# Performance work log

Measured on AMD Instinct MI355X. Metric: run time of the kernel, lower is better.

Reference implementation:

```python
import jax, jax.numpy as jnp
import numpy as np

# ---- config constants (must match init_kwargs) ----
B, S, D, H, HD = 2, 2048, 512, 8, 64
N_BLK, L_BLK = 64, 32          # block_size, block_len (S = N_BLK*L_BLK)
R, RM = 8, 4                   # router_size, group_router_mul_factor
LN, GN, GE, GT = 8, 4, 16, 2   # moe layers, groups, group experts, topk per token
DR, DG = 128, 128
FFH = 1024
THETA = 10000.0
EPS = 1e-6

_INV_FREQ = (1.0 / THETA) ** (np.arange(0, HD, 2, dtype=np.float32) / HD)


def rmsnorm(x, w):
    return x * jax.lax.rsqrt(jnp.mean(x * x, axis=-1, keepdims=True) + EPS) * w


def rope(x):
    # x: (b, h, s, hd); y1 = x1*cos + x2*sin, y2 = -x1*sin + x2*cos (as in RotaryEmb)
    s = x.shape[2]
    freqs = jnp.outer(jnp.arange(s, dtype=jnp.float32), jnp.asarray(_INV_FREQ))[None, None]
    cos, sin = jnp.cos(freqs), jnp.sin(freqs)
    x1, x2 = jnp.split(x, 2, axis=-1)
    return jnp.concatenate([x1 * cos + x2 * sin, -x1 * sin + x2 * cos], axis=-1)


def layer(x, mask, qkv_w, o_w, up_w, down_w, n1, n2):
    b, s, d = x.shape
    xn = rmsnorm(x, n1)
    q, k, v = jnp.split(xn @ qkv_w, 3, axis=-1)
    sh = lambda t: t.reshape(b, s, H, HD).transpose(0, 2, 1, 3)  # b h s hd
    q, k, v = rope(sh(q)), rope(sh(k)), sh(v)
    scores = jnp.einsum('bhqa,bhka->bhqk', q, k) / np.sqrt(HD).astype(np.float32)
    if mask is not None:
        scores = jnp.where(mask[:, None], scores, -jnp.inf)
    p = jax.nn.softmax(scores, axis=-1)
    o = jnp.einsum('bhqk,bhka->bhqa', p, v).transpose(0, 2, 1, 3).reshape(b, s, d)
    x = x + o @ o_w
    xn2 = rmsnorm(x, n2)
    h1, h2 = jnp.split(xn2 @ up_w, 2, axis=-1)
    return x + (jax.nn.silu(h1) * h2) @ down_w


def _l2n(t, axis):
    return t / jnp.maximum(jnp.linalg.norm(t, axis=axis, keepdims=True), 1e-12)


def forward(x, doc, router_token, out_w, keys_router, keys_gate,
            enc_qkv, enc_o, enc_up, enc_down, enc_n1, enc_n2,
            rtr_qkv, rtr_o, rtr_up, rtr_down, rtr_n1, rtr_n2):
    # ---- AuxEncoder: block-causal AND same-document mask (global_attn branch) ----
    qb = jnp.arange(S) // N_BLK
    causal = qb[:, None] >= qb[None, :]                       # (S, S)
    mask = causal[None] & (doc[:, :, None] == doc[:, None, :])  # (B, S, S)
    for i in range(enc_qkv.shape[0]):
        x = layer(x, mask, enc_qkv[i], enc_o[i], enc_up[i], enc_down[i], enc_n1[i], enc_n2[i])

    # ---- AuxRouter: split into blocks, append router tokens, full attention ----
    xr = x.reshape(B * L_BLK, N_BLK, D)
    rt = jnp.broadcast_to(router_token, (B * L_BLK, R, D))
    xr = jnp.concatenate([xr, rt], axis=1)                    # (B*L, N+R, D)
    for i in range(rtr_qkv.shape[0]):
        xr = layer(xr, None, rtr_qkv[i], rtr_o[i], rtr_up[i], rtr_down[i], rtr_n1[i], rtr_n2[i])
    out = xr[:, N_BLK:] @ out_w                               # (B*L, R, DR+DG)
    xro, xgo = out[..., :DR], out[..., DR:]

    def expand(t, dd):
        # repeat '(b l) r d -> (r rm) b l d', roll(1, dim=2), flatten(1,2)
        t = t.reshape(B, L_BLK, R, dd).transpose(2, 0, 1, 3)  # (R, B, L, d)
        t = jnp.repeat(t, RM, axis=0)                          # (R*RM, B, L, d)
        t = jnp.roll(t, 1, axis=2)
        return t.reshape(R * RM, B * L_BLK, dd)

    xrr = _l2n(expand(xro, DR), -1)
    xgg = _l2n(expand(xgo, DG), -1)
    kr = _l2n(keys_router, 1)
    kg = _l2n(keys_gate, 1)
    rl = jnp.einsum('gbd,gde->gbe', xrr, kr)                  # (LN*GN, B*L, GE)
    gl = jnp.einsum('gbd,gde->gbe', xgg, kg)
    _, idx = jax.lax.top_k(rl, GT)                            # (LN*GN, B*L, GT)
    rv = jnp.take_along_axis(rl, idx, axis=-1)
    gv = jnp.take_along_axis(gl, idx, axis=-1)
    return jnp.stack([rv, gv], axis=0)                        # (2, 32, 64, 2)


def setup_inputs() -> dict:
    key = jax.random.key(0)
    ks = jax.random.split(key, 20)
    w = lambda k, shp: 0.02 * jax.random.normal(k, shp, dtype=jnp.float32)
    return {
        'x': jax.random.normal(ks[0], (B, S, D), dtype=jnp.float32),
        'doc': jnp.sort(jax.random.randint(ks[1], (B, S), 0, 4), axis=-1),
        'router_token': jax.random.normal(ks[2], (1, R, D), dtype=jnp.float32),
        'out_w': w(ks[3], (D, DR + DG)),
        'keys_router': jax.random.normal(ks[4], (LN * GN, DR, GE), dtype=jnp.float32),
        'keys_gate': jax.random.normal(ks[5], (LN * GN, DG, GE), dtype=jnp.float32),
        'enc_qkv': w(ks[6], (4, D, 3 * D)),
        'enc_o': w(ks[7], (4, D, D)),
        'enc_up': w(ks[8], (4, D, 2 * FFH)),
        'enc_down': w(ks[9], (4, FFH, D)),
        'enc_n1': jnp.ones((4, D), dtype=jnp.float32),
        'enc_n2': jnp.ones((4, D), dtype=jnp.float32),
        'rtr_qkv': w(ks[10], (2, D, 3 * D)),
        'rtr_o': w(ks[11], (2, D, D)),
        'rtr_up': w(ks[12], (2, D, 2 * FFH)),
        'rtr_down': w(ks[13], (2, FFH, D)),
        'rtr_n1': jnp.ones((2, D), dtype=jnp.float32),
        'rtr_n2': jnp.ones((2, D), dtype=jnp.float32),
    }


def reference(x, doc, router_token, out_w, keys_router, keys_gate,
              enc_qkv, enc_o, enc_up, enc_down, enc_n1, enc_n2,
              rtr_qkv, rtr_o, rtr_up, rtr_down, rtr_n1, rtr_n2):
    return forward(x, doc, router_token, out_w, keys_router, keys_gate,
                   enc_qkv, enc_o, enc_up, enc_down, enc_n1, enc_n2,
                   rtr_qkv, rtr_o, rtr_up, rtr_down, rtr_n1, rtr_n2)
```

## Files before the change

### kernel.cpp

```cpp
#include <hip/hip_runtime.h>
#include <hip/hip_bf16.h>
#include <cstdint>


typedef __attribute__((ext_vector_type(8))) short short8;
typedef __attribute__((ext_vector_type(4))) float f32x4;
typedef unsigned short ushort_t;

__device__ __forceinline__ float bf2f(unsigned short u) {
    return __uint_as_float(((unsigned)u) << 16);
}
__device__ __forceinline__ unsigned short f2bf(float f) {
    unsigned u = __float_as_uint(f);
    unsigned r = 0x7FFFu + ((u >> 16) & 1u);
    return (unsigned short)((u + r) >> 16);
}
__device__ __forceinline__ float wave_sum64(float v) {
#pragma unroll
    for (int o = 32; o; o >>= 1) v += __shfl_xor(v, o);
    return v;
}
__device__ __forceinline__ void load_lds16(const ushort_t* g, ushort_t* l) {
    __builtin_amdgcn_global_load_lds(
        (const __attribute__((address_space(1))) unsigned int*)g,
        (__attribute__((address_space(3))) unsigned int*)l, 16, 0, 0);
}

#define MFMA16(a, b, c) __builtin_amdgcn_mfma_f32_16x16x32_bf16(a, b, c, 0, 0, 0)

__global__ void copy_in_kernel(const float* __restrict__ src,
                               float* __restrict__ dst, int n) {
    int i = blockIdx.x * 256 + threadIdx.x;
    if (i < n) dst[i] = src[i];
}

__global__ __launch_bounds__(256) void wsplit_kernel(const float* __restrict__ W,
        unsigned short* __restrict__ WH, unsigned short* __restrict__ WL,
        int K, int N) {
    __shared__ float tile[32][33];
    int bn = blockIdx.x * 32, bk = blockIdx.y * 32;
    int tx = threadIdx.x & 31, ty = threadIdx.x >> 5;
#pragma unroll
    for (int i = 0; i < 4; ++i)
        tile[ty + 8 * i][tx] = W[(size_t)(bk + ty + 8 * i) * N + bn + tx];
    __syncthreads();
#pragma unroll
    for (int i = 0; i < 4; ++i) {
        int n = bn + ty + 8 * i, k = bk + tx;
        float x = tile[tx][ty + 8 * i];
        unsigned short h = f2bf(x);
        unsigned short lo = f2bf(x - bf2f(h));
        WH[(size_t)n * K + k] = h;
        WL[(size_t)n * K + k] = lo;
    }
}

__global__ __launch_bounds__(256) void rmsnorm_kernel(const float* __restrict__ X,
        const float* __restrict__ W, ushort_t* __restrict__ XNH,
        ushort_t* __restrict__ XNL) {
    int t = blockIdx.x, tid = threadIdx.x;
    const float* xr = X + (size_t)t * 512;
    float v0 = xr[tid], v1 = xr[tid + 256];
    float ss = wave_sum64(v0 * v0 + v1 * v1);
    __shared__ float red[4];
    if ((tid & 63) == 0) red[tid >> 6] = ss;
    __syncthreads();
    float tot = red[0] + red[1] + red[2] + red[3];
    float scale = rsqrtf(tot * (1.0f / 512.0f) + 1e-6f);
    float a0 = v0 * scale * W[tid];
    float a1 = v1 * scale * W[tid + 256];
    unsigned short h0 = f2bf(a0), h1 = f2bf(a1);
    size_t base = (size_t)t * 512;
    XNH[base + tid]       = h0;
    XNL[base + tid]       = f2bf(a0 - bf2f(h0));
    XNH[base + tid + 256] = h1;
    XNL[base + tid + 256] = f2bf(a1 - bf2f(h1));
}

template <int BM>
__global__ __launch_bounds__(256) void gemm3(
        const ushort_t* __restrict__ AH, const ushort_t* __restrict__ AL,
        const ushort_t* __restrict__ BH, const ushort_t* __restrict__ BL,
        const float* __restrict__ Res, float* __restrict__ C,
        int M, int N, int K) {
    constexpr int MI  = BM / 32;
    constexpr int NLA = BM / 16;
    __shared__ __align__(16) ushort_t Ah[2][BM][32];
    __shared__ __align__(16) ushort_t Al[2][BM][32];
    __shared__ __align__(16) ushort_t Bh[2][128][32];
    __shared__ __align__(16) ushort_t Bl[2][128][32];
    int tid = threadIdx.x;
    int n0 = blockIdx.x * 128, m0 = blockIdx.y * BM;
    int wid = tid >> 6, lane = tid & 63;
    int wm = (wid >> 1) * (BM / 2), wn = (wid & 1) * 64;
    int col = lane & 15, quad = lane >> 4;

    const ushort_t* gb;
    ushort_t* lb0;
    int bstep, nl;
    if (wid == 0)      { gb = AH + (size_t)m0 * K; lb0 = &Ah[0][0][0]; bstep = BM * 32;  nl = NLA; }
    else if (wid == 1) { gb = AL + (size_t)m0 * K; lb0 = &Al[0][0][0]; bstep = BM * 32;  nl = NLA; }
    else if (wid == 2) { gb = BH + (size_t)n0 * K; lb0 = &Bh[0][0][0]; bstep = 128 * 32; nl = 8; }
    else               { gb = BL + (size_t)n0 * K; lb0 = &Bl[0][0][0]; bstep = 128 * 32; nl = 8; }
    const ushort_t* gsrc = gb + (size_t)(lane >> 2) * K
                              + (size_t)(((lane & 3) ^ ((lane >> 3) & 3)) * 8);

    auto STAGE = [&](int b, int kc) {
        const ushort_t* gs = gsrc + kc * 32;
        ushort_t* lb = lb0 + (size_t)b * bstep;
#pragma unroll
        for (int p = 0; p < 8; ++p)
            if (p < nl) load_lds16(gs + (size_t)(p * 16) * K, lb + p * 512);
    };

    int chrd = (quad ^ ((col >> 1) & 3)) * 8;
    f32x4 acc[MI][4] = {};
    int nk = K >> 5;
    STAGE(0, 0);
    __syncthreads();
    int cur = 0;
#pragma unroll 1
    for (int kc = 0; kc < nk; ++kc) {
        if (kc + 1 < nk) STAGE(cur ^ 1, kc + 1);
        short8 afh[MI], afl[MI], bfh[4], bfl[4];
#pragma unroll
        for (int i = 0; i < MI; ++i) {
            afh[i] = *(const short8*)&Ah[cur][wm + i * 16 + col][chrd];
            afl[i] = *(const short8*)&Al[cur][wm + i * 16 + col][chrd];
        }
#pragma unroll
        for (int i = 0; i < 4; ++i) {
            bfh[i] = *(const short8*)&Bh[cur][wn + i * 16 + col][chrd];
            bfl[i] = *(const short8*)&Bl[cur][wn + i * 16 + col][chrd];
        }
#pragma unroll
        for (int mi = 0; mi < MI; ++mi)
#pragma unroll
            for (int ni = 0; ni < 4; ++ni) {
                f32x4 c = acc[mi][ni];
                c = MFMA16(afh[mi], bfh[ni], c);
                c = MFMA16(afh[mi], bfl[ni], c);
                c = MFMA16(afl[mi], bfh[ni], c);
                acc[mi][ni] = c;
            }
        __syncthreads();
        cur ^= 1;
    }
#pragma unroll
    for (int mi = 0; mi < MI; ++mi)
#pragma unroll
        for (int ni = 0; ni < 4; ++ni)
#pragma unroll
            for (int r = 0; r < 4; ++r) {
                int row = m0 + wm + mi * 16 + quad * 4 + r;
                int ccol = n0 + wn + ni * 16 + col;
                size_t o = (size_t)row * N + ccol;
                float v = acc[mi][ni][r];
                if (Res) v += Res[o];
                C[o] = v;
            }
}

__global__ void rope_pack_kernel(const float* __restrict__ QKV,
        float* __restrict__ Q, ushort_t* __restrict__ KH,
        ushort_t* __restrict__ KL, int Sg, int total) {
    int idx = blockIdx.x * 256 + threadIdx.x;
    if (idx >= total) return;
    int i = idx & 31;
    int h = (idx >> 5) & 7;
    int t = idx >> 8;
    int g = t / Sg; int s = t - g * Sg;
    const float* row = QKV + (size_t)t * 1536;
    float inv = powf(10000.0f, -(float)(2 * i) / 64.0f);
    float sn, cs;
    sincosf((float)s * inv, &sn, &cs);
    size_t ob = ((size_t)(g * 8 + h) * Sg + s) * 64 + i;
    int c = h * 64 + i;
    float q1 = row[c], q2 = row[c + 32];
    Q[ob]      = q1 * cs + q2 * sn;
    Q[ob + 32] = q2 * cs - q1 * sn;
    float k1 = row[512 + c], k2 = row[512 + c + 32];
    float ka = k1 * cs + k2 * sn;
    float kb = k2 * cs - k1 * sn;
    unsigned short ha = f2bf(ka), hb = f2bf(kb);
    KH[ob]      = ha;  KL[ob]      = f2bf(ka - bf2f(ha));
    KH[ob + 32] = hb;  KL[ob + 32] = f2bf(kb - bf2f(hb));
}

__global__ __launch_bounds__(256) void vtrans_kernel(const float* __restrict__ QKV,
        ushort_t* __restrict__ VTH, ushort_t* __restrict__ VTL, int Sg) {
    __shared__ float tile[64][65];
    int chunk = blockIdx.x, gh = blockIdx.y;
    int g = gh >> 3, h = gh & 7;
    int tid = threadIdx.x;
    int sr = tid >> 2, dc = (tid & 3) * 16;
    int s = chunk * 64 + sr;
    if (s < Sg) {
        const float* src = QKV + ((size_t)g * Sg + s) * 1536 + 1024 + h * 64 + dc;
#pragma unroll
        for (int j = 0; j < 4; ++j) {
            float4 v = *(const float4*)(src + 4 * j);
            tile[sr][dc + 4 * j]     = v.x;
            tile[sr][dc + 4 * j + 1] = v.y;
            tile[sr][dc + 4 * j + 2] = v.z;
            tile[sr][dc + 4 * j + 3] = v.w;
        }
    } else {
#pragma unroll
        for (int j = 0; j < 16; ++j) tile[sr][dc + j] = 0.f;
    }
    __syncthreads();
    int dr = tid >> 2, sc = (tid & 3) * 16;
    short8 hv[2], lv[2];
#pragma unroll
    for (int half = 0; half < 2; ++half)
#pragma unroll
        for (int j = 0; j < 8; ++j) {
            float v = tile[sc + half * 8 + j][dr];
            unsigned short hb = f2bf(v);
            hv[half][j] = (short)hb;
            lv[half][j] = (short)f2bf(v - bf2f(hb));
        }
    int scol = chunk * 64 + sc;
    size_t ob = ((size_t)gh * 64 + dr) * Sg + scol;
    if (scol + 16 <= Sg) {
        *(short8*)(VTH + ob)     = hv[0];
        *(short8*)(VTH + ob + 8) = hv[1];
        *(short8*)(VTL + ob)     = lv[0];
        *(short8*)(VTL + ob + 8) = lv[1];
    } else {
#pragma unroll
        for (int j = 0; j < 16; ++j)
            if (scol + j < Sg) {
                VTH[ob + j] = (ushort_t)((j < 8) ? hv[0][j] : hv[1][j - 8]);
                VTL[ob + j] = (ushort_t)((j < 8) ? lv[0][j] : lv[1][j - 8]);
            }
    }
}

template <bool MASKED>
__global__ __launch_bounds__(256, 3) void attn3_kernel(const float* __restrict__ Q,
        const ushort_t* __restrict__ KHg, const ushort_t* __restrict__ KLg,
        const ushort_t* __restrict__ VTHg, const ushort_t* __restrict__ VTLg,
        const int* __restrict__ doc, ushort_t* __restrict__ AOH,
        ushort_t* __restrict__ AOL, int Sg) {
    __shared__ __align__(16) ushort_t Khs[64][64], Kls[64][64];
    __shared__ __align__(16) ushort_t Vts[64][64], Vtl[64][64];
    __shared__ __align__(16) ushort_t Ph[4][16][72], Pl[4][16][72];
    __shared__ int dock[64];
    int qb = (int)(gridDim.x - 1 - blockIdx.x);
    int gh = blockIdx.y, g = gh >> 3;
    int tid = threadIdx.x, wid = tid >> 6, lane = tid & 63;
    int col = lane & 15, quad = lane >> 4;

    int rL = lane >> 3, cSw = (lane & 7) ^ rL;
    const ushort_t* kb;
    const ushort_t* vb;
    ushort_t* lb;
    if (wid == 0)      { kb = KHg + (size_t)gh * Sg * 64 + cSw * 8;  vb = nullptr; lb = &Khs[0][0]; }
    else if (wid == 1) { kb = KLg + (size_t)gh * Sg * 64 + cSw * 8;  vb = nullptr; lb = &Kls[0][0]; }
    else if (wid == 2) { vb = VTHg + ((size_t)gh * 64 + rL) * Sg;    kb = nullptr; lb = &Vts[0][0]; }
    else               { vb = VTLg + ((size_t)gh * 64 + rL) * Sg;    kb = nullptr; lb = &Vtl[0][0]; }
    int sw0 = ((0 + quad) ^ (col & 7)) * 8;
    int sw1 = ((4 + quad) ^ (col & 7)) * 8;

    short8 qa[2][2];
    {
        int qrow = qb * 64 + wid * 16 + col;
        if (qrow >= Sg) qrow = Sg - 1;
        const float* Qg = Q + ((size_t)gh * Sg + qrow) * 64 + quad * 8;
#pragma unroll
        for (int kk = 0; kk < 2; ++kk) {
            float4 v0 = *(const float4*)(Qg + kk * 32);
            float4 v1 = *(const float4*)(Qg + kk * 32 + 4);
            float vv[8] = {v0.x, v0.y, v0.z, v0.w, v1.x, v1.y, v1.z, v1.w};
            short8 h, l;
#pragma unroll
            for (int e = 0; e < 8; ++e) {
                float x = vv[e] * 0.125f;
                unsigned short hb = f2bf(x);
                h[e] = (short)hb;
                l[e] = (short)f2bf(x - bf2f(hb));
            }
            qa[kk][0] = h; qa[kk][1] = l;
        }
    }
    int dqr[4]; int wq0 = 0, wq1 = 0, bq0 = 0, bq1 = 0;
    if (MASKED) {
        const int* db = doc + (size_t)g * Sg + qb * 64;
#pragma unroll
        for (int r = 0; r < 4; ++r) dqr[r] = db[wid * 16 + quad * 4 + r];
        wq0 = db[wid * 16]; wq1 = db[wid * 16 + 15];
        bq0 = db[0];        bq1 = db[63];
    }
    float m[4], l[4];
    f32x4 accO[4];
#pragma unroll
    for (int r = 0; r < 4; ++r) { m[r] = -1e30f; l[r] = 0.f; }
#pragma unroll
    for (int nd = 0; nd < 4; ++nd) accO[nd] = (f32x4){0.f, 0.f, 0.f, 0.f};

    int nkt = MASKED ? (qb + 1) : ((Sg + 63) >> 6);
    for (int kt = 0; kt < nkt; ++kt) {
        int kval = Sg - kt * 64; if (kval > 64) kval = 64;
        __syncthreads();
        if (MASKED) {
            if (tid < 64) dock[tid] = doc[(size_t)g * Sg + kt * 64 + tid];
            __syncthreads();
        }
        bool bskip = false;
        if (MASKED) bskip = (dock[63] < bq0) || (dock[0] > bq1);
        if (!bskip) {
            if (wid < 2) {
#pragma unroll
                for (int p = 0; p < 8; ++p) {
                    int sr2 = kt * 64 + p * 8 + rL;
                    if (sr2 > Sg - 1) sr2 = Sg - 1;
                    load_lds16(kb + (size_t)sr2 * 64, lb + p * 512);
                }
            } else {
                int vc = kt * 64 + cSw * 8;
                if (vc > Sg - 8) vc = Sg - 8;
#pragma unroll
                for (int p = 0; p < 8; ++p)
                    load_lds16(vb + (size_t)(p * 8) * Sg + vc, lb + p * 512);
            }
            __syncthreads();
            bool wskip = false;
            if (MASKED) wskip = (dock[kval - 1] < wq0) || (dock[0] > wq1);
            if (!wskip) {
                int dk[4];
                if (MASKED) {
#pragma unroll
                    for (int ni = 0; ni < 4; ++ni) dk[ni] = dock[ni * 16 + col];
                }
                f32x4 sc[4];
#pragma unroll
                for (int ni = 0; ni < 4; ++ni) {
                    int rb = (ni * 16 + col) * 64;
                    short8 bh0 = *(const short8*)(&Khs[0][0] + rb + sw0);
                    short8 bl0 = *(const short8*)(&Kls[0][0] + rb + sw0);
                    short8 bh1 = *(const short8*)(&Khs[0][0] + rb + sw1);
                    short8 bl1 = *(const short8*)(&Kls[0][0] + rb + sw1);
                    f32x4 c = (f32x4){0.f, 0.f, 0.f, 0.f};
                    c = MFMA16(qa[0][0], bh0, c);
                    c = MFMA16(qa[0][0], bl0, c);
                    c = MFMA16(qa[0][1], bh0, c);
                    c = MFMA16(qa[1][0], bh1, c);
                    c = MFMA16(qa[1][0], bl1, c);
                    c = MFMA16(qa[1][1], bh1, c);
                    sc[ni] = c;
                }
                float mnew[4];
#pragma unroll
                for (int r = 0; r < 4; ++r) mnew[r] = -1e30f;
#pragma unroll
                for (int ni = 0; ni < 4; ++ni)
#pragma unroll
                    for (int r = 0; r < 4; ++r) {
                        bool ok = MASKED ? (dk[ni] == dqr[r]) : (ni * 16 + col < kval);
                        float s = ok ? sc[ni][r] : -1e30f;
                        sc[ni][r] = s;
                        mnew[r] = fmaxf(mnew[r], s);
                    }
#pragma unroll
                for (int r = 0; r < 4; ++r)
#pragma unroll
                    for (int o = 1; o < 16; o <<= 1)
                        mnew[r] = fmaxf(mnew[r], __shfl_xor(mnew[r], o));
                float alpha[4], lsum[4];
#pragma unroll
                for (int r = 0; r < 4; ++r) {
                    float M = fmaxf(m[r], mnew[r]);
                    alpha[r] = __expf(m[r] - M);
                    m[r] = M;
                    lsum[r] = 0.f;
                }
#pragma unroll
                for (int ni = 0; ni < 4; ++ni)
#pragma unroll
                    for (int r = 0; r < 4; ++r) {
                        bool ok = MASKED ? (dk[ni] == dqr[r]) : (ni * 16 + col < kval);
                        float p = ok ? __expf(sc[ni][r] - m[r]) : 0.f;
                        lsum[r] += p;
                        unsigned short h = f2bf(p);
                        Ph[wid][quad * 4 + r][ni * 16 + col] = h;
                        Pl[wid][quad * 4 + r][ni * 16 + col] = f2bf(p - bf2f(h));
                    }
#pragma unroll
                for (int r = 0; r < 4; ++r) {
#pragma unroll
                    for (int o = 1; o < 16; o <<= 1)
                        lsum[r] += __shfl_xor(lsum[r], o);
                    l[r] = l[r] * alpha[r] + lsum[r];
                }
#pragma unroll
                for (int nd = 0; nd < 4; ++nd)
#pragma unroll
                    for (int r = 0; r < 4; ++r) accO[nd][r] *= alpha[r];
#pragma unroll
                for (int kk = 0; kk < 2; ++kk) {
                    short8 pah = *(const short8*)&Ph[wid][col][kk * 32 + quad * 8];
                    short8 pal = *(const short8*)&Pl[wid][col][kk * 32 + quad * 8];
                    int sw = kk ? sw1 : sw0;
#pragma unroll
                    for (int nd = 0; nd < 4; ++nd) {
                        int rb = (nd * 16 + col) * 64;
                        short8 vbh = *(const short8*)(&Vts[0][0] + rb + sw);
                        short8 vbl = *(const short8*)(&Vtl[0][0] + rb + sw);
                        f32x4 c = accO[nd];
                        c = MFMA16(pah, vbh, c);
                        c = MFMA16(pah, vbl, c);
                        c = MFMA16(pal, vbh, c);
                        accO[nd] = c;
                    }
                }
            }
        }
    }
#pragma unroll
    for (int r = 0; r < 4; ++r) {
        int qrow = qb * 64 + wid * 16 + quad * 4 + r;
        if (qrow < Sg) {
            float inv = 1.0f / l[r];
            size_t base = ((size_t)g * Sg + qrow) * 512 + (gh & 7) * 64;
#pragma unroll
            for (int nd = 0; nd < 4; ++nd) {
                float val = accO[nd][r] * inv;
                unsigned short h = f2bf(val);
                AOH[base + nd * 16 + col] = h;
                AOL[base + nd * 16 + col] = f2bf(val - bf2f(h));
            }
        }
    }
}

__global__ void silu_mul_kernel(const float* __restrict__ H,
        ushort_t* __restrict__ MIDH, ushort_t* __restrict__ MIDL, int total) {
    int idx = blockIdx.x * 256 + threadIdx.x;
    if (idx >= total) return;
    int t = idx >> 10, j = idx & 1023;
    float a = H[(size_t)t * 2048 + j];
    float b = H[(size_t)t * 2048 + 1024 + j];
    float r = (a / (1.0f + __expf(-a))) * b;
    unsigned short h = f2bf(r);
    MIDH[idx] = h;
    MIDL[idx] = f2bf(r - bf2f(h));
}

__global__ void router_build_kernel(const float* __restrict__ X,
        const float* __restrict__ RT, float* __restrict__ X2, int total) {
    int idx = blockIdx.x * 256 + threadIdx.x;
    if (idx >= total) return;
    int d = idx & 511;
    int p = (idx >> 9) % 72;
    int g2 = idx / (72 * 512);
    X2[idx] = (p < 64) ? X[((size_t)g2 * 64 + p) * 512 + d]
                       : RT[(p - 64) * 512 + d];
}

__global__ void gather_rows_kernel(const float* __restrict__ X2,
        ushort_t* __restrict__ RRH, ushort_t* __restrict__ RRL, int total) {
    int idx = blockIdx.x * 256 + threadIdx.x;
    if (idx >= total) return;
    int d = idx & 511;
    int row = idx >> 9;
    int g2 = row >> 3, rr = row & 7;
    float v = X2[((size_t)(g2 * 72 + 64 + rr)) * 512 + d];
    unsigned short h = f2bf(v);
    RRH[idx] = h;
    RRL[idx] = f2bf(v - bf2f(h));
}

__global__ __launch_bounds__(64) void norm_half_kernel(const float* __restrict__ IN,
        float* __restrict__ OUT) {
    int b = blockIdx.x; int lane = threadIdx.x;
    size_t base = (size_t)(b >> 1) * 256 + (size_t)(b & 1) * 128;
    float v0 = IN[base + lane], v1 = IN[base + 64 + lane];
    float ss = wave_sum64(v0 * v0 + v1 * v1);
    float sc = 1.0f / fmaxf(sqrtf(ss), 1e-12f);
    OUT[base + lane]      = v0 * sc;
    OUT[base + 64 + lane] = v1 * sc;
}

__global__ __launch_bounds__(64) void norm_keys_kernel(const float* __restrict__ Kin,
        float* __restrict__ Kout) {
    int b = blockIdx.x; int lane = threadIdx.x;
    int g = b >> 4, e = b & 15;
    size_t base = (size_t)g * 2048 + e;
    float v0 = Kin[base + (size_t)lane * 16];
    float v1 = Kin[base + (size_t)(lane + 64) * 16];
    float ss = wave_sum64(v0 * v0 + v1 * v1);
    float sc = 1.0f / fmaxf(sqrtf(ss), 1e-12f);
    Kout[base + (size_t)lane * 16]        = v0 * sc;
    Kout[base + (size_t)(lane + 64) * 16] = v1 * sc;
}

__global__ __launch_bounds__(64) void logits_top2_kernel(const float* __restrict__ OUTN,
        const float* __restrict__ KRN, const float* __restrict__ KGN,
        float* __restrict__ out) {
    int blk = blockIdx.x;
    int g = blk >> 6, bcol = blk & 63;
    int b = bcol >> 5, l = bcol & 31;
    int lsrc = (l + 31) & 31;
    int r = g >> 2;
    int row = (b * 32 + lsrc) * 8 + r;
    const float* rvec = OUTN + (size_t)row * 256;
    __shared__ float sc[32];
    int lane = threadIdx.x;
    if (lane < 32) {
        int e = lane & 15;
        const float* kb = ((lane < 16) ? KRN : KGN) + (size_t)g * 2048 + e;
        const float* xv = (lane < 16) ? rvec : (rvec + 128);
        float s = 0.f;
#pragma unroll 8
        for (int d = 0; d < 128; ++d) s = fmaf(xv[d], kb[(size_t)d * 16], s);
        sc[lane] = s;
    }
    __syncthreads();
    if (lane == 0) {
        float bv = -1e30f, sv = -1e30f; int bi = 0, si = 0;
#pragma unroll
        for (int e = 0; e < 16; ++e) {
            float v = sc[e];
            if (v > bv) { sv = bv; si = bi; bv = v; bi = e; }
            else if (v > sv) { sv = v; si = e; }
        }
        size_t base = (size_t)g * 128 + (size_t)bcol * 2;
        out[base]            = bv;
        out[base + 1]        = sv;
        out[4096 + base]     = sc[16 + bi];
        out[4096 + base + 1] = sc[16 + si];
    }
}

static void run_layer(float* X, float* BIG, float* Qb,
                      ushort_t* KHb, ushort_t* KLb, ushort_t* VTHb, ushort_t* VTLb,
                      ushort_t* XNH, ushort_t* XNL, ushort_t* AOH, ushort_t* AOL,
                      ushort_t* MIDH, ushort_t* MIDL,
                      const unsigned short* WH, const unsigned short* WL,
                      const float* n1, const float* n2,
                      const int* doc, int G, int Sg, hipStream_t stream) {
    const size_t oQKV = 0, oO = 786432, oUP = 1048576, oDN = 2097152;
    int T = G * Sg;
    rmsnorm_kernel<<<T, 256, 0, stream>>>(X, n1, XNH, XNL);
    gemm3<128><<<dim3(12, T / 128), 256, 0, stream>>>(XNH, XNL, WH + oQKV, WL + oQKV, nullptr, BIG, T, 1536, 512);
    int rp = T * 256;
    rope_pack_kernel<<<(rp + 255) / 256, 256, 0, stream>>>(BIG, Qb, KHb, KLb, Sg, rp);
    int qblocks = (Sg + 63) >> 6;
    vtrans_kernel<<<dim3(qblocks, G * 8), 256, 0, stream>>>(BIG, VTHb, VTLb, Sg);
    if (doc)
        attn3_kernel<true><<<dim3(qblocks, G * 8), 256, 0, stream>>>(Qb, KHb, KLb, VTHb, VTLb, doc, AOH, AOL, Sg);
    else
        attn3_kernel<false><<<dim3(qblocks, G * 8), 256, 0, stream>>>(Qb, KHb, KLb, VTHb, VTLb, nullptr, AOH, AOL, Sg);
    gemm3<64><<<dim3(4, T / 64), 256, 0, stream>>>(AOH, AOL, WH + oO, WL + oO, X, X, T, 512, 512);
    rmsnorm_kernel<<<T, 256, 0, stream>>>(X, n2, XNH, XNL);
    gemm3<128><<<dim3(16, T / 128), 256, 0, stream>>>(XNH, XNL, WH + oUP, WL + oUP, nullptr, BIG, T, 2048, 512);
    silu_mul_kernel<<<(T * 1024 + 255) / 256, 256, 0, stream>>>(BIG, MIDH, MIDL, T * 1024);
    gemm3<64><<<dim3(4, T / 64), 256, 0, stream>>>(MIDH, MIDL, WH + oDN, WL + oDN, X, X, T, 512, 1024);
}

static void split_layer(const float* qkv, const float* o, const float* up, const float* dn,
                        unsigned short* WH, unsigned short* WL, hipStream_t stream) {
    const size_t oQKV = 0, oO = 786432, oUP = 1048576, oDN = 2097152;
    wsplit_kernel<<<dim3(48, 16), 256, 0, stream>>>(qkv, WH + oQKV, WL + oQKV, 512, 1536);
    wsplit_kernel<<<dim3(16, 16), 256, 0, stream>>>(o,   WH + oO,   WL + oO,   512, 512);
    wsplit_kernel<<<dim3(64, 16), 256, 0, stream>>>(up,  WH + oUP,  WL + oUP,  512, 2048);
    wsplit_kernel<<<dim3(16, 32), 256, 0, stream>>>(dn,  WH + oDN,  WL + oDN,  1024, 512);
}

extern "C" void kernel_launch(void* const* d_in, const int* in_sizes, int n_in,
                              void* d_out, int out_size, void* d_ws, size_t ws_size,
                              hipStream_t stream) {
    const float* x_in    = (const float*)d_in[0];
    const int*   doc     = (const int*)d_in[1];
    const float* rt      = (const float*)d_in[2];
    const float* out_w   = (const float*)d_in[3];
    const float* k_rt    = (const float*)d_in[4];
    const float* k_gt    = (const float*)d_in[5];
    const float* enc_qkv = (const float*)d_in[6];
    const float* enc_o   = (const float*)d_in[7];
    const float* enc_up  = (const float*)d_in[8];
    const float* enc_dn  = (const float*)d_in[9];
    const float* enc_n1  = (const float*)d_in[10];
    const float* enc_n2  = (const float*)d_in[11];
    const float* rtr_qkv = (const float*)d_in[12];
    const float* rtr_o   = (const float*)d_in[13];
    const float* rtr_up  = (const float*)d_in[14];
    const float* rtr_dn  = (const float*)d_in[15];
    const float* rtr_n1  = (const float*)d_in[16];
    const float* rtr_n2  = (const float*)d_in[17];

    float* ws = (float*)d_ws;
    size_t off = 0;
    auto alloc = [&](size_t n) { float* p = ws + off; off += n; return p; };
    float* X    = alloc(4608UL * 512);
    float* X2   = alloc(4608UL * 512);
    float* BIG  = alloc(4608UL * 2048);
    float* Qb   = alloc(4608UL * 512);
    ushort_t* KHb  = (ushort_t*)alloc(1179648UL);
    ushort_t* KLb  = (ushort_t*)alloc(1179648UL);
    ushort_t* VTHb = (ushort_t*)alloc(1179648UL);
    ushort_t* VTLb = (ushort_t*)alloc(1179648UL);
    unsigned short* WH = (unsigned short*)(ws + off);
    unsigned short* WL = WH + 2621440UL;
    off += 2621440UL;
    ushort_t* XNH = (ushort_t*)Qb;
    ushort_t* XNL = XNH + 4608UL * 512;
    ushort_t* MIDH = (ushort_t*)Qb;
    ushort_t* MIDL = (ushort_t*)KHb;
    ushort_t* AOH = (ushort_t*)BIG;
    ushort_t* AOL = AOH + 4608UL * 512;
    ushort_t* RRH = (ushort_t*)X;
    ushort_t* RRL = RRH + 262144;
    float* OUTM = X + 262144;
    float* OUTN = X + 393216;
    float* KRN  = X + 524288;
    float* KGN  = X + 589824;
    (void)ws_size; (void)in_sizes; (void)n_in; (void)out_size;

    copy_in_kernel<<<(2097152 + 255) / 256, 256, 0, stream>>>(x_in, X, 2097152);

    for (int i = 0; i < 4; ++i) {
        split_layer(enc_qkv + (size_t)i * 512 * 1536,
                    enc_o   + (size_t)i * 512 * 512,
                    enc_up  + (size_t)i * 512 * 2048,
                    enc_dn  + (size_t)i * 1024 * 512, WH, WL, stream);
        run_layer(X, BIG, Qb, KHb, KLb, VTHb, VTLb, XNH, XNL, AOH, AOL, MIDH, MIDL,
                  WH, WL, enc_n1 + (size_t)i * 512, enc_n2 + (size_t)i * 512,
                  doc, 2, 2048, stream);
    }

    int rb_total = 64 * 72 * 512;
    router_build_kernel<<<(rb_total + 255) / 256, 256, 0, stream>>>(X, rt, X2, rb_total);

    for (int i = 0; i < 2; ++i) {
        split_layer(rtr_qkv + (size_t)i * 512 * 1536,
                    rtr_o   + (size_t)i * 512 * 512,
                    rtr_up  + (size_t)i * 512 * 2048,
                    rtr_dn  + (size_t)i * 1024 * 512, WH, WL, stream);
        run_layer(X2, BIG, Qb, KHb, KLb, VTHb, VTLb, XNH, XNL, AOH, AOL, MIDH, MIDL,
                  WH, WL, rtr_n1 + (size_t)i * 512, rtr_n2 + (size_t)i * 512,
                  nullptr, 64, 72, stream);
    }

    gather_rows_kernel<<<(512 * 512) / 256, 256, 0, stream>>>(X2, RRH, RRL, 512 * 512);
    wsplit_kernel<<<dim3(8, 16), 256, 0, stream>>>(out_w, WH, WL, 512, 256);
    gemm3<64><<<dim3(2, 8), 256, 0, stream>>>(RRH, RRL, WH, WL, nullptr, OUTM, 512, 256, 512);

    norm_half_kernel<<<1024, 64, 0, stream>>>(OUTM, OUTN);
    norm_keys_kernel<<<512, 64, 0, stream>>>(k_rt, KRN);
    norm_keys_kernel<<<512, 64, 0, stream>>>(k_gt, KGN);
    logits_top2_kernel<<<2048, 64, 0, stream>>>(OUTN, KRN, KGN, (float*)d_out);
}
```

Measured before the change: 1.446 ms.

## Triple-buffer GEMM LDS staging with manual vmcnt waits and smaller M tiles

```diff
diff --git a/kernel.cpp b/kernel.cpp
--- a/kernel.cpp
+++ b/kernel.cpp
@@ -27,6 +27,8 @@
 }
 
 #define MFMA16(a, b, c) __builtin_amdgcn_mfma_f32_16x16x32_bf16(a, b, c, 0, 0, 0)
+#define BARRIER_RAW() do { asm volatile("" ::: "memory"); \
+    __builtin_amdgcn_s_barrier(); asm volatile("" ::: "memory"); } while (0)
 
 __global__ void copy_in_kernel(const float* __restrict__ src,
                                float* __restrict__ dst, int n) {
@@ -83,55 +85,65 @@
         const ushort_t* __restrict__ BH, const ushort_t* __restrict__ BL,
         const float* __restrict__ Res, float* __restrict__ C,
         int M, int N, int K) {
-    constexpr int MI  = BM / 32;
-    constexpr int NLA = BM / 16;
-    __shared__ __align__(16) ushort_t Ah[2][BM][32];
-    __shared__ __align__(16) ushort_t Al[2][BM][32];
-    __shared__ __align__(16) ushort_t Bh[2][128][32];
-    __shared__ __align__(16) ushort_t Bl[2][128][32];
+    constexpr int MI   = BM / 32;
+    constexpr int ROWS = 2 * BM + 256;
+    constexpr int LPW  = ROWS / 64;
+    constexpr int SS   = ROWS * 32;
+    __shared__ __align__(16) ushort_t S[3][ROWS][32];
     int tid = threadIdx.x;
     int n0 = blockIdx.x * 128, m0 = blockIdx.y * BM;
     int wid = tid >> 6, lane = tid & 63;
     int wm = (wid >> 1) * (BM / 2), wn = (wid & 1) * 64;
     int col = lane & 15, quad = lane >> 4;
 
-    const ushort_t* gb;
-    ushort_t* lb0;
-    int bstep, nl;
-    if (wid == 0)      { gb = AH + (size_t)m0 * K; lb0 = &Ah[0][0][0]; bstep = BM * 32;  nl = NLA; }
-    else if (wid == 1) { gb = AL + (size_t)m0 * K; lb0 = &Al[0][0][0]; bstep = BM * 32;  nl = NLA; }
-    else if (wid == 2) { gb = BH + (size_t)n0 * K; lb0 = &Bh[0][0][0]; bstep = 128 * 32; nl = 8; }
-    else               { gb = BL + (size_t)n0 * K; lb0 = &Bl[0][0][0]; bstep = 128 * 32; nl = 8; }
-    const ushort_t* gsrc = gb + (size_t)(lane >> 2) * K
-                              + (size_t)(((lane & 3) ^ ((lane >> 3) & 3)) * 8);
-
-    auto STAGE = [&](int b, int kc) {
-        const ushort_t* gs = gsrc + kc * 32;
-        ushort_t* lb = lb0 + (size_t)b * bstep;
-#pragma unroll
-        for (int p = 0; p < 8; ++p)
-            if (p < nl) load_lds16(gs + (size_t)(p * 16) * K, lb + p * 512);
+    const ushort_t* gsrc[LPW];
+    int ldof[LPW];
+#pragma unroll
+    for (int j = 0; j < LPW; ++j) {
+        int e = wid * LPW + j;
+        int srow = e * 16 + (lane >> 2);
+        const ushort_t* gp; int rin;
+        if (srow < BM)                { gp = AH + (size_t)m0 * K; rin = srow; }
+        else if (srow < 2 * BM)       { gp = AL + (size_t)m0 * K; rin = srow - BM; }
+        else if (srow < 2 * BM + 128) { gp = BH + (size_t)n0 * K; rin = srow - 2 * BM; }
+        else                          { gp = BL + (size_t)n0 * K; rin = srow - 2 * BM - 128; }
+        gsrc[j] = gp + (size_t)rin * K + ((lane & 3) ^ ((lane >> 3) & 3)) * 8;
+        ldof[j] = e * 512;
+    }
+    ushort_t* sbase = &S[0][0][0];
+    auto STAGE = [&](int set, int kc) {
+        ushort_t* sb = sbase + set * SS;
+#pragma unroll
+        for (int j = 0; j < LPW; ++j)
+            load_lds16(gsrc[j] + kc * 32, sb + ldof[j]);
+    };
+    auto WAITK = [&]() {
+        if constexpr (BM == 64) asm volatile("s_waitcnt vmcnt(6)" ::: "memory");
+        else                    asm volatile("s_waitcnt vmcnt(8)" ::: "memory");
     };
 
     int chrd = (quad ^ ((col >> 1) & 3)) * 8;
     f32x4 acc[MI][4] = {};
     int nk = K >> 5;
     STAGE(0, 0);
-    __syncthreads();
-    int cur = 0;
+    if (nk > 1) { STAGE(1, 1); WAITK(); }
+    else        { asm volatile("s_waitcnt vmcnt(0)" ::: "memory"); }
+    BARRIER_RAW();
+    int sc = 0, sn = 1, sp = 2;
 #pragma unroll 1
     for (int kc = 0; kc < nk; ++kc) {
-        if (kc + 1 < nk) STAGE(cur ^ 1, kc + 1);
+        if (kc + 2 < nk) STAGE(sp, kc + 2);
+        const ushort_t* sb = sbase + sc * SS;
         short8 afh[MI], afl[MI], bfh[4], bfl[4];
 #pragma unroll
         for (int i = 0; i < MI; ++i) {
-            afh[i] = *(const short8*)&Ah[cur][wm + i * 16 + col][chrd];
-            afl[i] = *(const short8*)&Al[cur][wm + i * 16 + col][chrd];
+            afh[i] = *(const short8*)(sb + (size_t)(wm + i * 16 + col) * 32 + chrd);
+            afl[i] = *(const short8*)(sb + (size_t)(BM + wm + i * 16 + col) * 32 + chrd);
         }
 #pragma unroll
         for (int i = 0; i < 4; ++i) {
-            bfh[i] = *(const short8*)&Bh[cur][wn + i * 16 + col][chrd];
-            bfl[i] = *(const short8*)&Bl[cur][wn + i * 16 + col][chrd];
+            bfh[i] = *(const short8*)(sb + (size_t)(2 * BM + wn + i * 16 + col) * 32 + chrd);
+            bfl[i] = *(const short8*)(sb + (size_t)(2 * BM + 128 + wn + i * 16 + col) * 32 + chrd);
         }
 #pragma unroll
         for (int mi = 0; mi < MI; ++mi)
@@ -143,8 +155,12 @@
                 c = MFMA16(afl[mi], bfh[ni], c);
                 acc[mi][ni] = c;
             }
-        __syncthreads();
-        cur ^= 1;
+        if (kc + 1 < nk) {
+            if (kc + 2 < nk) WAITK();
+            else asm volatile("s_waitcnt vmcnt(0)" ::: "memory");
+            BARRIER_RAW();
+        }
+        int t = sc; sc = sn; sn = sp; sp = t;
     }
 #pragma unroll
     for (int mi = 0; mi < MI; ++mi)
@@ -544,7 +560,7 @@
     const size_t oQKV = 0, oO = 786432, oUP = 1048576, oDN = 2097152;
     int T = G * Sg;
     rmsnorm_kernel<<<T, 256, 0, stream>>>(X, n1, XNH, XNL);
-    gemm3<128><<<dim3(12, T / 128), 256, 0, stream>>>(XNH, XNL, WH + oQKV, WL + oQKV, nullptr, BIG, T, 1536, 512);
+    gemm3<64><<<dim3(12, T / 64), 256, 0, stream>>>(XNH, XNL, WH + oQKV, WL + oQKV, nullptr, BIG, T, 1536, 512);
     int rp = T * 256;
     rope_pack_kernel<<<(rp + 255) / 256, 256, 0, stream>>>(BIG, Qb, KHb, KLb, Sg, rp);
     int qblocks = (Sg + 63) >> 6;
@@ -555,7 +571,7 @@
         attn3_kernel<false><<<dim3(qblocks, G * 8), 256, 0, stream>>>(Qb, KHb, KLb, VTHb, VTLb, nullptr, AOH, AOL, Sg);
     gemm3<64><<<dim3(4, T / 64), 256, 0, stream>>>(AOH, AOL, WH + oO, WL + oO, X, X, T, 512, 512);
     rmsnorm_kernel<<<T, 256, 0, stream>>>(X, n2, XNH, XNL);
-    gemm3<128><<<dim3(16, T / 128), 256, 0, stream>>>(XNH, XNL, WH + oUP, WL + oUP, nullptr, BIG, T, 2048, 512);
+    gemm3<64><<<dim3(16, T / 64), 256, 0, stream>>>(XNH, XNL, WH + oUP, WL + oUP, nullptr, BIG, T, 2048, 512);
     silu_mul_kernel<<<(T * 1024 + 255) / 256, 256, 0, stream>>>(BIG, MIDH, MIDL, T * 1024);
     gemm3<64><<<dim3(4, T / 64), 256, 0, stream>>>(MIDH, MIDL, WH + oDN, WL + oDN, X, X, T, 512, 1024);
 }
```

Result: faster. 1.371 ms (-5.2%).
